# Kernel optimization log

Measured on AMD Instinct MI355X. Metric: run time of the kernel, lower is better.

The kernel has to match this reference:

```python
import jax, jax.numpy as jnp
import numpy as np
import math

# IPA hyperparameters (AlphaFold2 / ProtSeed defaults)
H, C, PQ, PV = 12, 16, 4, 8
CS, CZ = 384, 128
INF, EPS = 1e5, 1e-8
CAT = H * (CZ + C + 4 * PV)  # 2112


def setup_inputs() -> dict:
    key = jax.random.key(0)
    ks = jax.random.split(key, 20)
    B, N = 1, 512
    s = jax.random.normal(ks[0], (B, N, CS), jnp.float32)
    z = jax.random.normal(ks[1], (B, N, N, CZ), jnp.float32)
    # valid rotation matrices via QR of random gaussians
    rot = jnp.linalg.qr(jax.random.normal(ks[2], (B, N, 3, 3), jnp.float32))[0]
    trans = jax.random.normal(ks[3], (B, N, 3), jnp.float32)
    mask = jnp.ones((B, N), jnp.float32)
    sc = 0.02
    params = {
        'w_q': jax.random.normal(ks[4], (CS, H * C), jnp.float32) * sc,
        'b_q': jnp.zeros((H * C,), jnp.float32),
        'w_kv': jax.random.normal(ks[5], (CS, 2 * H * C), jnp.float32) * sc,
        'b_kv': jnp.zeros((2 * H * C,), jnp.float32),
        'w_qp': jax.random.normal(ks[6], (CS, H * PQ * 3), jnp.float32) * sc,
        'b_qp': jnp.zeros((H * PQ * 3,), jnp.float32),
        'w_kvp': jax.random.normal(ks[7], (CS, H * (PQ + PV) * 3), jnp.float32) * sc,
        'b_kvp': jnp.zeros((H * (PQ + PV) * 3,), jnp.float32),
        'w_b': jax.random.normal(ks[8], (CZ, H), jnp.float32) * sc,
        'b_b': jnp.zeros((H,), jnp.float32),
        'head_weights': jnp.full((H,), 0.5414, jnp.float32),  # softplus^-1(1)
        'w_out': jax.random.normal(ks[9], (CAT, CS), jnp.float32) * sc,
        'b_out': jnp.zeros((CS,), jnp.float32),
    }
    return {'s': s, 'z': z, 'rot': rot, 'trans': trans, 'mask': mask, **params}


def reference(s, z, rot, trans, mask, w_q, b_q, w_kv, b_kv, w_qp, b_qp,
              w_kvp, b_kvp, w_b, b_b, head_weights, w_out, b_out):
    B, N, _ = s.shape
    w_c = math.sqrt(1.0 / (3 * C))
    w_l = math.sqrt(1.0 / 3)
    w_p = math.sqrt(1.0 / (3 * (PQ * 9.0 / 2)))

    # scalar q/k/v: [B,N,H,C]
    q = (s @ w_q + b_q).reshape(B, N, H, C)
    kv = (s @ w_kv + b_kv).reshape(B, N, H, 2 * C)
    k, v = kv[..., :C], kv[..., C:]

    # point q/k/v in global frame. torch splits the projection into 3 chunks
    # (x,y,z) along the channel dim then stacks -> [B,N,H*P,3]
    def to_pts(w, b, p):
        pts = jnp.stack(jnp.split(s @ w + b, 3, axis=-1), axis=-1)  # [B,N,H*p,3]
        pts = jnp.einsum('bnij,bnpj->bnpi', rot, pts) + trans[:, :, None, :]
        return pts.reshape(B, N, H, p, 3)

    q_pts = to_pts(w_qp, b_qp, PQ)
    kv_pts = to_pts(w_kvp, b_kvp, PQ + PV)
    k_pts, v_pts = kv_pts[..., :PQ, :], kv_pts[..., PQ:, :]

    # pair bias [B,N,N,H]
    bias = z @ w_b + b_b

    # scalar attention logits [B,H,i,j]
    a = jnp.einsum('bihc,bjhc->bhij', q, k) * w_c
    a = a + w_l * jnp.transpose(bias, (0, 3, 1, 2))

    # point-distance term: [B,i,j,H,PQ]
    d2 = jnp.sum((q_pts[:, :, None] - k_pts[:, None]) ** 2, axis=-1)
    hw = jax.nn.softplus(head_weights) * w_p
    pt_att = -0.5 * jnp.sum(d2 * hw[None, None, None, :, None], axis=-1)  # [B,i,j,H]
    a = a + jnp.transpose(pt_att, (0, 3, 1, 2))

    sq_mask = INF * (mask[:, :, None] * mask[:, None, :] - 1.0)  # [B,i,j]
    a = jax.nn.softmax(a + sq_mask[:, None], axis=-1)  # [B,H,i,j]

    # scalar output [B,N,H*C]
    o = jnp.einsum('bhij,bjhc->bihc', a, v).reshape(B, N, H * C)

    # point output, mapped back to local frames: [B,i,H,PV,3]
    o_pt = jnp.einsum('bhij,bjhpx->bihpx', a, v_pts)
    o_pt = jnp.einsum('bnji,bnhpj->bnhpi', rot, o_pt - trans[:, :, None, None, :])
    o_pt_norm = jnp.sqrt(jnp.sum(o_pt ** 2, axis=-1) + EPS).reshape(B, N, H * PV)
    o_pt = o_pt.reshape(B, N, H * PV, 3)

    # pair output [B,N,H*CZ]
    o_pair = jnp.einsum('bhij,bijc->bihc', a, z).reshape(B, N, H * CZ)

    cat = jnp.concatenate(
        [o, o_pt[..., 0], o_pt[..., 1], o_pt[..., 2], o_pt_norm, o_pair], axis=-1)
    return cat @ w_out + b_out  # [B,N,C_s]
```

## Files before the change

### kernel.cpp

```cpp
#include <hip/hip_runtime.h>
#include <math.h>

#define NN 512
#define CSd 384
#define CATd 2112
#define KF_CHUNK 264
#define KF_SPLIT 8

__device__ __forceinline__ int aidx(int h, int j) {
  return h * 544 + ((j >> 6) * 68) + (j & 63);
}
__device__ __forceinline__ float f4c(const float4& v, int k) {
  return k == 0 ? v.x : (k == 1 ? v.y : (k == 2 ? v.z : v.w));
}

__global__ void k_projgemm(const float* __restrict__ s,
                           const float* __restrict__ w_q, const float* __restrict__ b_q,
                           const float* __restrict__ w_kv, const float* __restrict__ b_kv,
                           const float* __restrict__ w_qp, const float* __restrict__ b_qp,
                           const float* __restrict__ w_kvp, const float* __restrict__ b_kvp,
                           float* __restrict__ proj)
{
  __shared__ float sT[384 * 40];
  const int t  = threadIdx.x;
  const int i0 = blockIdx.x * 32;
  const int c0 = blockIdx.y * 64;

  for (int u = t; u < 32 * 384; u += 256) {
    int row = u / 384, col = u % 384;
    sT[col * 40 + row] = s[(i0 + row) * CSd + col];
  }
  __syncthreads();

  const int c    = t & 63;
  const int rgrp = t >> 6;
  const int gc   = c0 + c;

  const float* wp;
  int stride;
  float bias;
  if (gc < 192)      { wp = w_q   + gc;         stride = 192; bias = b_q[gc]; }
  else if (gc < 576) { wp = w_kv  + (gc - 192); stride = 384; bias = b_kv[gc - 192]; }
  else if (gc < 720) { wp = w_qp  + (gc - 576); stride = 144; bias = b_qp[gc - 576]; }
  else               { wp = w_kvp + (gc - 720); stride = 432; bias = b_kvp[gc - 720]; }

  float acc[8];
#pragma unroll
  for (int j = 0; j < 8; j++) acc[j] = bias;

  const int r0 = rgrp * 8;
#pragma unroll 4
  for (int kk = 0; kk < 384; kk++) {
    float wv = *wp; wp += stride;
    const float4 a0 = *reinterpret_cast<const float4*>(&sT[kk * 40 + r0]);
    const float4 a1 = *reinterpret_cast<const float4*>(&sT[kk * 40 + r0 + 4]);
    acc[0] += a0.x * wv; acc[1] += a0.y * wv; acc[2] += a0.z * wv; acc[3] += a0.w * wv;
    acc[4] += a1.x * wv; acc[5] += a1.y * wv; acc[6] += a1.z * wv; acc[7] += a1.w * wv;
  }
#pragma unroll
  for (int j = 0; j < 8; j++)
    proj[(size_t)(i0 + r0 + j) * 1152 + gc] = acc[j];
}

__global__ void k_rot(const float* __restrict__ proj,
                      const float* __restrict__ rot, const float* __restrict__ trans,
                      float* __restrict__ q, float* __restrict__ kT, float* __restrict__ vcat,
                      float* __restrict__ qp, float* __restrict__ kpT)
{
  __shared__ float ptsL[576];
  const int i = blockIdx.x, t = threadIdx.x;
  const float* pr = proj + (size_t)i * 1152;

  for (int u = t; u < 576; u += 256) ptsL[u] = pr[576 + u];

  for (int cI = t; cI < 576; cI += 256) {
    float pv = pr[cI];
    if (cI < 192) q[i * 192 + cI] = pv;
    else {
      int local = cI - 192, h = local >> 5, cc = local & 31;
      if (cc < 16) kT[(size_t)(h * 16 + cc) * NN + i] = pv;
      else         vcat[(size_t)i * 480 + h * 16 + (cc - 16)] = pv;
    }
  }
  __syncthreads();

  for (int p = t; p < 192; p += 256) {
    float x, y, zz;
    if (p < 48) { x = ptsL[p]; y = ptsL[48 + p]; zz = ptsL[96 + p]; }
    else { int idx = p - 48; x = ptsL[144 + idx]; y = ptsL[288 + idx]; zz = ptsL[432 + idx]; }
    const float* Rm = rot + i * 9;
    const float* tr = trans + i * 3;
    float rx = Rm[0] * x + Rm[1] * y + Rm[2] * zz + tr[0];
    float ry = Rm[3] * x + Rm[4] * y + Rm[5] * zz + tr[1];
    float rz = Rm[6] * x + Rm[7] * y + Rm[8] * zz + tr[2];
    if (p < 48) {
      float* d = qp + ((size_t)i * 48 + p) * 3;
      d[0] = rx; d[1] = ry; d[2] = rz;
    } else {
      int idx = p - 48, h = idx / 12, pp = idx % 12;
      if (pp < 4) {
        size_t rbase = (size_t)((h * 4 + pp) * 3) * NN + i;
        kpT[rbase] = rx; kpT[rbase + NN] = ry; kpT[rbase + 2 * NN] = rz;
      } else {
        size_t rbase = (size_t)i * 480 + 192 + (h * 8 + pp - 4) * 3;
        vcat[rbase] = rx; vcat[rbase + 1] = ry; vcat[rbase + 2] = rz;
      }
    }
  }
}

__global__ void k_logits(const float* __restrict__ z, const float* __restrict__ w_b,
                         const float* __restrict__ b_b, const float* __restrict__ mask,
                         const float* __restrict__ q, const float* __restrict__ kT,
                         const float* __restrict__ qp, const float* __restrict__ kpT,
                         const float* __restrict__ hws,
                         float* __restrict__ a)
{
  const int t = threadIdx.x;
  const int i = blockIdx.x >> 1;
  const int j = ((blockIdx.x & 1) << 8) + t;

  float acc[12];
#pragma unroll
  for (int h = 0; h < 12; h++) acc[h] = 0.f;

  const float4* zr = reinterpret_cast<const float4*>(z + ((size_t)i * NN + j) * 128);
#pragma unroll
  for (int ch = 0; ch < 4; ch++) {
    float4 zc[8];
#pragma unroll
    for (int u = 0; u < 8; u++) zc[u] = zr[ch * 8 + u];
#pragma unroll
    for (int u = 0; u < 8; u++) {
      const int c0 = ch * 32 + u * 4;
#pragma unroll
      for (int h = 0; h < 12; h++) {
        acc[h] += zc[u].x * w_b[(c0 + 0) * 12 + h]
                + zc[u].y * w_b[(c0 + 1) * 12 + h]
                + zc[u].z * w_b[(c0 + 2) * 12 + h]
                + zc[u].w * w_b[(c0 + 3) * 12 + h];
      }
    }
  }

  const float mterm = 100000.0f * (mask[i] * mask[j] - 1.0f);
  const float W_L = 0.57735026919f;
  const float W_C = 0.14433756730f;

#pragma unroll
  for (int h = 0; h < 12; h++) {
    float dot = 0.f;
#pragma unroll
    for (int c = 0; c < 16; c++)
      dot += q[i * 192 + h * 16 + c] * kT[(size_t)(h * 16 + c) * NN + j];
    float d2 = 0.f;
#pragma unroll
    for (int pc = 0; pc < 12; pc++) {
      float dd = qp[(size_t)i * 144 + h * 12 + pc] - kpT[(size_t)(h * 12 + pc) * NN + j];
      d2 += dd * dd;
    }
    const float hwv = 0.13608276348f * log1pf(expf(hws[h]));
    a[((size_t)h * NN + i) * NN + j] =
        W_L * (acc[h] + b_b[h]) + mterm + W_C * dot - 0.5f * hwv * d2;
  }
}

__global__ void __launch_bounds__(512, 2)
k_out(const float* __restrict__ a, const float* __restrict__ vcat,
      const float* __restrict__ z,
      const float* __restrict__ rot, const float* __restrict__ trans,
      float* __restrict__ cat)
{
  __shared__ float aL[12 * 544];
  __shared__ float redp[8][16][56];
  __shared__ float optF[288];
  float* red2 = &redp[0][0][0];

  const int i = blockIdx.x, t = threadIdx.x;

  for (int u = t; u < 12 * 512; u += 512) {
    int h = u >> 9, j = u & 511;
    aL[aidx(h, j)] = a[((size_t)h * NN + i) * NN + j];
  }
  __syncthreads();

  {
    const int wv = t >> 6, l = t & 63;
    for (int h = wv; h < 12; h += 8) {
      const int j0 = l * 8;
      float4 x0 = *reinterpret_cast<const float4*>(&aL[aidx(h, j0)]);
      float4 x1 = *reinterpret_cast<const float4*>(&aL[aidx(h, j0 + 4)]);
      float m8 = fmaxf(fmaxf(fmaxf(x0.x, x0.y), fmaxf(x0.z, x0.w)),
                       fmaxf(fmaxf(x1.x, x1.y), fmaxf(x1.z, x1.w)));
      for (int o = 1; o < 64; o <<= 1) m8 = fmaxf(m8, __shfl_xor(m8, o));
      x0.x = expf(x0.x - m8); x0.y = expf(x0.y - m8);
      x0.z = expf(x0.z - m8); x0.w = expf(x0.w - m8);
      x1.x = expf(x1.x - m8); x1.y = expf(x1.y - m8);
      x1.z = expf(x1.z - m8); x1.w = expf(x1.w - m8);
      float s8 = x0.x + x0.y + x0.z + x0.w + x1.x + x1.y + x1.z + x1.w;
      for (int o = 1; o < 64; o <<= 1) s8 += __shfl_xor(s8, o);
      float inv = 1.0f / s8;
      x0.x *= inv; x0.y *= inv; x0.z *= inv; x0.w *= inv;
      x1.x *= inv; x1.y *= inv; x1.z *= inv; x1.w *= inv;
      *reinterpret_cast<float4*>(&aL[aidx(h, j0)]) = x0;
      *reinterpret_cast<float4*>(&aL[aidx(h, j0 + 4)]) = x1;
    }
  }
  __syncthreads();

  const int cg = t & 15;
  const int jq = (t >> 4) & 3;
  const int wv = t >> 6;
  float acc1[12][8];
#pragma unroll
  for (int h = 0; h < 12; h++)
#pragma unroll
    for (int c = 0; c < 8; c++) acc1[h][c] = 0.f;

  {
    const int c8 = cg * 8;
    const int jb = wv * 64 + jq * 16;
    const float* zb = z + (size_t)i * 65536 + c8;
    for (int ch = 0; ch < 4; ch++) {
      const int j0c = jb + ch * 4;
      float4 p4[12];
#pragma unroll
      for (int h = 0; h < 12; h++)
        p4[h] = *reinterpret_cast<const float4*>(&aL[aidx(h, j0c)]);
#pragma unroll
      for (int jj = 0; jj < 4; jj++) {
        const float4 za = *reinterpret_cast<const float4*>(&zb[(size_t)(j0c + jj) * 128]);
        const float4 zc = *reinterpret_cast<const float4*>(&zb[(size_t)(j0c + jj) * 128 + 4]);
#pragma unroll
        for (int h = 0; h < 12; h++) {
          const float pv = f4c(p4[h], jj);
          acc1[h][0] += pv * za.x; acc1[h][1] += pv * za.y;
          acc1[h][2] += pv * za.z; acc1[h][3] += pv * za.w;
          acc1[h][4] += pv * zc.x; acc1[h][5] += pv * zc.y;
          acc1[h][6] += pv * zc.z; acc1[h][7] += pv * zc.w;
        }
      }
    }
#pragma unroll
    for (int h = 0; h < 12; h++)
#pragma unroll
      for (int c = 0; c < 8; c++) {
        float v2 = acc1[h][c];
        v2 += __shfl_xor(v2, 16);
        v2 += __shfl_xor(v2, 32);
        acc1[h][c] = v2;
      }
  }

  if (jq == 0) {
#pragma unroll
    for (int h = 0; h < 6; h++) {
      *reinterpret_cast<float4*>(&redp[wv][cg][h * 8]) =
        make_float4(acc1[h][0], acc1[h][1], acc1[h][2], acc1[h][3]);
      *reinterpret_cast<float4*>(&redp[wv][cg][h * 8 + 4]) =
        make_float4(acc1[h][4], acc1[h][5], acc1[h][6], acc1[h][7]);
    }
  }
  __syncthreads();
  for (int e = t; e < 768; e += 512) {
    int h = e >> 7, c = e & 127;
    float sv = 0.f;
#pragma unroll
    for (int w2 = 0; w2 < 8; w2++) sv += redp[w2][c >> 3][h * 8 + (c & 7)];
    cat[(size_t)i * CATd + 576 + e] = sv;
  }
  __syncthreads();

  if (jq == 0) {
#pragma unroll
    for (int h = 0; h < 6; h++) {
      *reinterpret_cast<float4*>(&redp[wv][cg][h * 8]) =
        make_float4(acc1[6 + h][0], acc1[6 + h][1], acc1[6 + h][2], acc1[6 + h][3]);
      *reinterpret_cast<float4*>(&redp[wv][cg][h * 8 + 4]) =
        make_float4(acc1[6 + h][4], acc1[6 + h][5], acc1[6 + h][6], acc1[6 + h][7]);
    }
  }
  __syncthreads();
  for (int e = t; e < 768; e += 512) {
    int h = e >> 7, c = e & 127;
    float sv = 0.f;
#pragma unroll
    for (int w2 = 0; w2 < 8; w2++) sv += redp[w2][c >> 3][h * 8 + (c & 7)];
    cat[(size_t)i * CATd + 576 + 768 + e] = sv;
  }
  __syncthreads();

  const int oc = t & 63, jw = t >> 6;
  const int h2 = oc / 5, c5 = oc - h2 * 5;
  const int c8b = c5 * 8;
  float acc2[8];
#pragma unroll
  for (int c = 0; c < 8; c++) acc2[c] = 0.f;

  if (oc < 60) {
    const int vbase = (c8b < 16) ? (h2 * 16 + c8b) : (192 + h2 * 24 + (c8b - 16));
    for (int ch = 0; ch < 16; ch++) {
      const int j0c = jw * 64 + ch * 4;
      const float4 p4 = *reinterpret_cast<const float4*>(&aL[aidx(h2, j0c)]);
#pragma unroll
      for (int jj = 0; jj < 4; jj++) {
        const float* vr = &vcat[(size_t)(j0c + jj) * 480 + vbase];
        const float4 va = *reinterpret_cast<const float4*>(vr);
        const float4 vb = *reinterpret_cast<const float4*>(vr + 4);
        const float pv = f4c(p4, jj);
        acc2[0] += pv * va.x; acc2[1] += pv * va.y;
        acc2[2] += pv * va.z; acc2[3] += pv * va.w;
        acc2[4] += pv * vb.x; acc2[5] += pv * vb.y;
        acc2[6] += pv * vb.z; acc2[7] += pv * vb.w;
      }
    }
  }
  if (oc < 60) {
    *reinterpret_cast<float4*>(&red2[((size_t)jw * 64 + oc) * 8]) =
      make_float4(acc2[0], acc2[1], acc2[2], acc2[3]);
    *reinterpret_cast<float4*>(&red2[((size_t)jw * 64 + oc) * 8 + 4]) =
      make_float4(acc2[4], acc2[5], acc2[6], acc2[7]);
  }
  __syncthreads();

  for (int e = t; e < 480; e += 512) {
    const int oc2 = e >> 3, cc = e & 7;
    float sv = 0.f;
#pragma unroll
    for (int w2 = 0; w2 < 8; w2++) sv += red2[((size_t)w2 * 64 + oc2) * 8 + cc];
    const int hh = e / 40, c40 = e - hh * 40;
    if (c40 < 16) cat[(size_t)i * CATd + hh * 16 + c40] = sv;
    else optF[hh * 24 + (c40 - 16)] = sv;
  }
  __syncthreads();

  if (t < 96) {
    const int h = t >> 3, p = t & 7;
    const float* Rm = rot + i * 9;
    const float* tr = trans + i * 3;
    float ox = optF[h * 24 + p * 3 + 0] - tr[0];
    float oy = optF[h * 24 + p * 3 + 1] - tr[1];
    float oz = optF[h * 24 + p * 3 + 2] - tr[2];
    float rx = Rm[0] * ox + Rm[3] * oy + Rm[6] * oz;
    float ry = Rm[1] * ox + Rm[4] * oy + Rm[7] * oz;
    float rz = Rm[2] * ox + Rm[5] * oy + Rm[8] * oz;
    float nrm = sqrtf(rx * rx + ry * ry + rz * rz + 1e-8f);
    size_t b = (size_t)i * CATd;
    cat[b + 192 + t] = rx; cat[b + 288 + t] = ry;
    cat[b + 384 + t] = rz; cat[b + 480 + t] = nrm;
  }
}

__global__ void k_final(const float* __restrict__ cat, const float* __restrict__ w_out,
                        float* __restrict__ part)
{
  __shared__ float sT[KF_CHUNK * 36];
  const int t  = threadIdx.x;
  const int i0 = blockIdx.x * 32;
  const int c0 = blockIdx.y * 64;
  const int k0 = blockIdx.z * KF_CHUNK;

  for (int u = t; u < 32 * KF_CHUNK; u += 256) {
    int row = u / KF_CHUNK, kk = u % KF_CHUNK;
    sT[kk * 36 + row] = cat[(size_t)(i0 + row) * CATd + k0 + kk];
  }
  __syncthreads();

  const int c    = t & 63;
  const int rgrp = t >> 6;
  const int r0   = rgrp * 8;
  const int gc   = c0 + c;

  float acc[8];
#pragma unroll
  for (int j = 0; j < 8; j++) acc[j] = 0.f;

  const float* wp = w_out + (size_t)k0 * 384 + gc;
#pragma unroll 4
  for (int kk = 0; kk < KF_CHUNK; kk++) {
    float wv = wp[(size_t)kk * 384];
    const float4 a0 = *reinterpret_cast<const float4*>(&sT[kk * 36 + r0]);
    const float4 a1 = *reinterpret_cast<const float4*>(&sT[kk * 36 + r0 + 4]);
    acc[0] += a0.x * wv; acc[1] += a0.y * wv; acc[2] += a0.z * wv; acc[3] += a0.w * wv;
    acc[4] += a1.x * wv; acc[5] += a1.y * wv; acc[6] += a1.z * wv; acc[7] += a1.w * wv;
  }

  float* pb = part + (size_t)blockIdx.z * NN * 384;
#pragma unroll
  for (int j = 0; j < 8; j++)
    pb[(size_t)(i0 + r0 + j) * 384 + gc] = acc[j];
}

__global__ void k_reduce(const float* __restrict__ part, const float* __restrict__ b_out,
                         float* __restrict__ out)
{
  const int idx = blockIdx.x * 256 + threadIdx.x;
  const int c = idx % 384;
  float acc = b_out[c];
#pragma unroll
  for (int ks = 0; ks < KF_SPLIT; ks++)
    acc += part[(size_t)ks * NN * 384 + idx];
  out[idx] = acc;
}

extern "C" void kernel_launch(void* const* d_in, const int* in_sizes, int n_in,
                              void* d_out, int out_size, void* d_ws, size_t ws_size,
                              hipStream_t stream) {
  const float* s      = (const float*)d_in[0];
  const float* z      = (const float*)d_in[1];
  const float* rot    = (const float*)d_in[2];
  const float* trans  = (const float*)d_in[3];
  const float* mask   = (const float*)d_in[4];
  const float* w_q    = (const float*)d_in[5];
  const float* b_q    = (const float*)d_in[6];
  const float* w_kv   = (const float*)d_in[7];
  const float* b_kv   = (const float*)d_in[8];
  const float* w_qp   = (const float*)d_in[9];
  const float* b_qp   = (const float*)d_in[10];
  const float* w_kvp  = (const float*)d_in[11];
  const float* b_kvp  = (const float*)d_in[12];
  const float* w_b    = (const float*)d_in[13];
  const float* b_b    = (const float*)d_in[14];
  const float* hws    = (const float*)d_in[15];
  const float* w_out  = (const float*)d_in[16];
  const float* b_out  = (const float*)d_in[17];
  float* out = (float*)d_out;

  float* ws   = (float*)d_ws;
  float* q    = ws;
  float* kT   = q    + 98304;
  float* vcat = kT   + 98304;
  float* qp   = vcat + 245760;
  float* kpT  = qp   + 73728;
  float* a    = kpT  + 73728;
  float* cat  = a    + 3145728;
  float* proj = a;
  float* part = a;

  k_projgemm<<<dim3(16, 18), 256, 0, stream>>>(s, w_q, b_q, w_kv, b_kv,
                                               w_qp, b_qp, w_kvp, b_kvp, proj);
  k_rot<<<512, 256, 0, stream>>>(proj, rot, trans, q, kT, vcat, qp, kpT);
  k_logits<<<1024, 256, 0, stream>>>(z, w_b, b_b, mask, q, kT, qp, kpT, hws, a);
  k_out<<<512, 512, 0, stream>>>(a, vcat, z, rot, trans, cat);
  k_final<<<dim3(16, 6, KF_SPLIT), 256, 0, stream>>>(cat, w_out, part);
  k_reduce<<<768, 256, 0, stream>>>(part, b_out, out);
}
```

Baseline: 201.4 us.

## Split output kernel into softmax/value kernel and parallel pair-output kernel

The monolithic per-row output kernel is split in three. The first computes the softmax, writes the probabilities back to global memory and does the scalar and point value reductions against a transposed value layout. The second spreads the attention-by-z pair contraction over a 4x512 grid with a partial-sum buffer, and the third reduces those partials into the concat buffer. This aims to raise parallelism and occupancy on the z-bandwidth-bound pair product, at the cost of extra launches, an extra round trip of the attention matrix through global memory, and the partial-sum traffic.

```diff
diff --git a/kernel.cpp b/kernel.cpp
--- a/kernel.cpp
+++ b/kernel.cpp
@@ -6,13 +6,6 @@
 #define CATd 2112
 #define KF_CHUNK 264
 #define KF_SPLIT 8
-
-__device__ __forceinline__ int aidx(int h, int j) {
-  return h * 544 + ((j >> 6) * 68) + (j & 63);
-}
-__device__ __forceinline__ float f4c(const float4& v, int k) {
-  return k == 0 ? v.x : (k == 1 ? v.y : (k == 2 ? v.z : v.w));
-}
 
 __global__ void k_projgemm(const float* __restrict__ s,
                            const float* __restrict__ w_q, const float* __restrict__ b_q,
@@ -64,7 +57,7 @@
 
 __global__ void k_rot(const float* __restrict__ proj,
                       const float* __restrict__ rot, const float* __restrict__ trans,
-                      float* __restrict__ q, float* __restrict__ kT, float* __restrict__ vcat,
+                      float* __restrict__ q, float* __restrict__ kT, float* __restrict__ vcatT,
                       float* __restrict__ qp, float* __restrict__ kpT)
 {
   __shared__ float ptsL[576];
@@ -79,7 +72,7 @@
     else {
       int local = cI - 192, h = local >> 5, cc = local & 31;
       if (cc < 16) kT[(size_t)(h * 16 + cc) * NN + i] = pv;
-      else         vcat[(size_t)i * 480 + h * 16 + (cc - 16)] = pv;
+      else         vcatT[(size_t)(h * 16 + (cc - 16)) * NN + i] = pv;
     }
   }
   __syncthreads();
@@ -102,8 +95,8 @@
         size_t rbase = (size_t)((h * 4 + pp) * 3) * NN + i;
         kpT[rbase] = rx; kpT[rbase + NN] = ry; kpT[rbase + 2 * NN] = rz;
       } else {
-        size_t rbase = (size_t)i * 480 + 192 + (h * 8 + pp - 4) * 3;
-        vcat[rbase] = rx; vcat[rbase + 1] = ry; vcat[rbase + 2] = rz;
+        size_t rbase = (size_t)(192 + (h * 8 + pp - 4) * 3) * NN + i;
+        vcatT[rbase] = rx; vcatT[rbase + NN] = ry; vcatT[rbase + 2 * NN] = rz;
       }
     }
   }
@@ -165,172 +158,58 @@
   }
 }
 
-__global__ void __launch_bounds__(512, 2)
-k_out(const float* __restrict__ a, const float* __restrict__ vcat,
-      const float* __restrict__ z,
+__global__ void __launch_bounds__(512)
+k_pvt(float* __restrict__ a, const float* __restrict__ vcatT,
       const float* __restrict__ rot, const float* __restrict__ trans,
       float* __restrict__ cat)
 {
-  __shared__ float aL[12 * 544];
-  __shared__ float redp[8][16][56];
+  __shared__ float PL[12 * 516];
   __shared__ float optF[288];
-  float* red2 = &redp[0][0][0];
-
   const int i = blockIdx.x, t = threadIdx.x;
-
-  for (int u = t; u < 12 * 512; u += 512) {
-    int h = u >> 9, j = u & 511;
-    aL[aidx(h, j)] = a[((size_t)h * NN + i) * NN + j];
-  }
-  __syncthreads();
-
-  {
-    const int wv = t >> 6, l = t & 63;
-    for (int h = wv; h < 12; h += 8) {
-      const int j0 = l * 8;
-      float4 x0 = *reinterpret_cast<const float4*>(&aL[aidx(h, j0)]);
-      float4 x1 = *reinterpret_cast<const float4*>(&aL[aidx(h, j0 + 4)]);
-      float m8 = fmaxf(fmaxf(fmaxf(x0.x, x0.y), fmaxf(x0.z, x0.w)),
-                       fmaxf(fmaxf(x1.x, x1.y), fmaxf(x1.z, x1.w)));
-      for (int o = 1; o < 64; o <<= 1) m8 = fmaxf(m8, __shfl_xor(m8, o));
-      x0.x = expf(x0.x - m8); x0.y = expf(x0.y - m8);
-      x0.z = expf(x0.z - m8); x0.w = expf(x0.w - m8);
-      x1.x = expf(x1.x - m8); x1.y = expf(x1.y - m8);
-      x1.z = expf(x1.z - m8); x1.w = expf(x1.w - m8);
-      float s8 = x0.x + x0.y + x0.z + x0.w + x1.x + x1.y + x1.z + x1.w;
-      for (int o = 1; o < 64; o <<= 1) s8 += __shfl_xor(s8, o);
-      float inv = 1.0f / s8;
-      x0.x *= inv; x0.y *= inv; x0.z *= inv; x0.w *= inv;
-      x1.x *= inv; x1.y *= inv; x1.z *= inv; x1.w *= inv;
-      *reinterpret_cast<float4*>(&aL[aidx(h, j0)]) = x0;
-      *reinterpret_cast<float4*>(&aL[aidx(h, j0 + 4)]) = x1;
-    }
-  }
-  __syncthreads();
-
-  const int cg = t & 15;
-  const int jq = (t >> 4) & 3;
-  const int wv = t >> 6;
-  float acc1[12][8];
-#pragma unroll
-  for (int h = 0; h < 12; h++)
-#pragma unroll
-    for (int c = 0; c < 8; c++) acc1[h][c] = 0.f;
-
-  {
-    const int c8 = cg * 8;
-    const int jb = wv * 64 + jq * 16;
-    const float* zb = z + (size_t)i * 65536 + c8;
-    for (int ch = 0; ch < 4; ch++) {
-      const int j0c = jb + ch * 4;
-      float4 p4[12];
-#pragma unroll
-      for (int h = 0; h < 12; h++)
-        p4[h] = *reinterpret_cast<const float4*>(&aL[aidx(h, j0c)]);
-#pragma unroll
-      for (int jj = 0; jj < 4; jj++) {
-        const float4 za = *reinterpret_cast<const float4*>(&zb[(size_t)(j0c + jj) * 128]);
-        const float4 zc = *reinterpret_cast<const float4*>(&zb[(size_t)(j0c + jj) * 128 + 4]);
-#pragma unroll
-        for (int h = 0; h < 12; h++) {
-          const float pv = f4c(p4[h], jj);
-          acc1[h][0] += pv * za.x; acc1[h][1] += pv * za.y;
-          acc1[h][2] += pv * za.z; acc1[h][3] += pv * za.w;
-          acc1[h][4] += pv * zc.x; acc1[h][5] += pv * zc.y;
-          acc1[h][6] += pv * zc.z; acc1[h][7] += pv * zc.w;
-        }
-      }
-    }
-#pragma unroll
-    for (int h = 0; h < 12; h++)
-#pragma unroll
-      for (int c = 0; c < 8; c++) {
-        float v2 = acc1[h][c];
-        v2 += __shfl_xor(v2, 16);
-        v2 += __shfl_xor(v2, 32);
-        acc1[h][c] = v2;
-      }
-  }
-
-  if (jq == 0) {
-#pragma unroll
-    for (int h = 0; h < 6; h++) {
-      *reinterpret_cast<float4*>(&redp[wv][cg][h * 8]) =
-        make_float4(acc1[h][0], acc1[h][1], acc1[h][2], acc1[h][3]);
-      *reinterpret_cast<float4*>(&redp[wv][cg][h * 8 + 4]) =
-        make_float4(acc1[h][4], acc1[h][5], acc1[h][6], acc1[h][7]);
-    }
-  }
-  __syncthreads();
-  for (int e = t; e < 768; e += 512) {
-    int h = e >> 7, c = e & 127;
-    float sv = 0.f;
-#pragma unroll
-    for (int w2 = 0; w2 < 8; w2++) sv += redp[w2][c >> 3][h * 8 + (c & 7)];
-    cat[(size_t)i * CATd + 576 + e] = sv;
-  }
-  __syncthreads();
-
-  if (jq == 0) {
-#pragma unroll
-    for (int h = 0; h < 6; h++) {
-      *reinterpret_cast<float4*>(&redp[wv][cg][h * 8]) =
-        make_float4(acc1[6 + h][0], acc1[6 + h][1], acc1[6 + h][2], acc1[6 + h][3]);
-      *reinterpret_cast<float4*>(&redp[wv][cg][h * 8 + 4]) =
-        make_float4(acc1[6 + h][4], acc1[6 + h][5], acc1[6 + h][6], acc1[6 + h][7]);
-    }
-  }
-  __syncthreads();
-  for (int e = t; e < 768; e += 512) {
-    int h = e >> 7, c = e & 127;
-    float sv = 0.f;
-#pragma unroll
-    for (int w2 = 0; w2 < 8; w2++) sv += redp[w2][c >> 3][h * 8 + (c & 7)];
-    cat[(size_t)i * CATd + 576 + 768 + e] = sv;
-  }
-  __syncthreads();
-
-  const int oc = t & 63, jw = t >> 6;
-  const int h2 = oc / 5, c5 = oc - h2 * 5;
-  const int c8b = c5 * 8;
-  float acc2[8];
-#pragma unroll
-  for (int c = 0; c < 8; c++) acc2[c] = 0.f;
-
-  if (oc < 60) {
-    const int vbase = (c8b < 16) ? (h2 * 16 + c8b) : (192 + h2 * 24 + (c8b - 16));
-    for (int ch = 0; ch < 16; ch++) {
-      const int j0c = jw * 64 + ch * 4;
-      const float4 p4 = *reinterpret_cast<const float4*>(&aL[aidx(h2, j0c)]);
-#pragma unroll
-      for (int jj = 0; jj < 4; jj++) {
-        const float* vr = &vcat[(size_t)(j0c + jj) * 480 + vbase];
-        const float4 va = *reinterpret_cast<const float4*>(vr);
-        const float4 vb = *reinterpret_cast<const float4*>(vr + 4);
-        const float pv = f4c(p4, jj);
-        acc2[0] += pv * va.x; acc2[1] += pv * va.y;
-        acc2[2] += pv * va.z; acc2[3] += pv * va.w;
-        acc2[4] += pv * vb.x; acc2[5] += pv * vb.y;
-        acc2[6] += pv * vb.z; acc2[7] += pv * vb.w;
-      }
-    }
-  }
-  if (oc < 60) {
-    *reinterpret_cast<float4*>(&red2[((size_t)jw * 64 + oc) * 8]) =
-      make_float4(acc2[0], acc2[1], acc2[2], acc2[3]);
-    *reinterpret_cast<float4*>(&red2[((size_t)jw * 64 + oc) * 8 + 4]) =
-      make_float4(acc2[4], acc2[5], acc2[6], acc2[7]);
-  }
-  __syncthreads();
-
-  for (int e = t; e < 480; e += 512) {
-    const int oc2 = e >> 3, cc = e & 7;
-    float sv = 0.f;
-#pragma unroll
-    for (int w2 = 0; w2 < 8; w2++) sv += red2[((size_t)w2 * 64 + oc2) * 8 + cc];
-    const int hh = e / 40, c40 = e - hh * 40;
-    if (c40 < 16) cat[(size_t)i * CATd + hh * 16 + c40] = sv;
-    else optF[hh * 24 + (c40 - 16)] = sv;
+  const int w = t >> 6, l = t & 63;
+
+  for (int u = t; u < 12 * 128; u += 512) {
+    int h = u >> 7, c4 = u & 127;
+    *reinterpret_cast<float4*>(&PL[h * 516 + c4 * 4]) =
+      *reinterpret_cast<const float4*>(&a[((size_t)h * NN + i) * NN + c4 * 4]);
+  }
+  __syncthreads();
+
+  for (int h = w; h < 12; h += 8) {
+    float x[8];
+    float m = -1e30f;
+#pragma unroll
+    for (int k = 0; k < 8; k++) { x[k] = PL[h * 516 + k * 64 + l]; m = fmaxf(m, x[k]); }
+    for (int o = 1; o < 64; o <<= 1) m = fmaxf(m, __shfl_xor(m, o));
+    float sm = 0.f;
+#pragma unroll
+    for (int k = 0; k < 8; k++) { x[k] = expf(x[k] - m); sm += x[k]; }
+    for (int o = 1; o < 64; o <<= 1) sm += __shfl_xor(sm, o);
+    float inv = 1.0f / sm;
+#pragma unroll
+    for (int k = 0; k < 8; k++) PL[h * 516 + k * 64 + l] = x[k] * inv;
+  }
+  __syncthreads();
+
+  for (int u = t; u < 12 * 128; u += 512) {
+    int h = u >> 7, c4 = u & 127;
+    *reinterpret_cast<float4*>(&a[((size_t)h * NN + i) * NN + c4 * 4]) =
+      *reinterpret_cast<const float4*>(&PL[h * 516 + c4 * 4]);
+  }
+
+  for (int v = w; v < 480; v += 8) {
+    const int h = (v < 192) ? (v >> 4) : ((v - 192) / 24);
+    const float* vr = vcatT + (size_t)v * NN;
+    const float* pr = PL + h * 516;
+    float acc = 0.f;
+#pragma unroll
+    for (int k = 0; k < 8; k++)
+      acc += pr[k * 64 + l] * vr[k * 64 + l];
+    for (int o = 1; o < 64; o <<= 1) acc += __shfl_xor(acc, o);
+    if (l == 0) {
+      if (v < 192) cat[(size_t)i * CATd + v] = acc;
+      else         optF[v - 192] = acc;
+    }
   }
   __syncthreads();
 
@@ -338,9 +217,9 @@
     const int h = t >> 3, p = t & 7;
     const float* Rm = rot + i * 9;
     const float* tr = trans + i * 3;
-    float ox = optF[h * 24 + p * 3 + 0] - tr[0];
-    float oy = optF[h * 24 + p * 3 + 1] - tr[1];
-    float oz = optF[h * 24 + p * 3 + 2] - tr[2];
+    float ox = optF[(h * 8 + p) * 3 + 0] - tr[0];
+    float oy = optF[(h * 8 + p) * 3 + 1] - tr[1];
+    float oz = optF[(h * 8 + p) * 3 + 2] - tr[2];
     float rx = Rm[0] * ox + Rm[3] * oy + Rm[6] * oz;
     float ry = Rm[1] * ox + Rm[4] * oy + Rm[7] * oz;
     float rz = Rm[2] * ox + Rm[5] * oy + Rm[8] * oz;
@@ -349,6 +228,60 @@
     cat[b + 192 + t] = rx; cat[b + 288 + t] = ry;
     cat[b + 384 + t] = rz; cat[b + 480 + t] = nrm;
   }
+}
+
+__global__ void k_opair(const float* __restrict__ a, const float* __restrict__ z,
+                        float* __restrict__ opart)
+{
+  __shared__ float PL[12 * 128];
+  __shared__ float red[4][64][26];
+  const int jb = blockIdx.x, i = blockIdx.y;
+  const int t = threadIdx.x, c2 = t & 63, jq = t >> 6;
+
+  for (int u = t; u < 384; u += 256) {
+    int h = u >> 5, c4 = u & 31;
+    *reinterpret_cast<float4*>(&PL[h * 128 + c4 * 4]) =
+      *reinterpret_cast<const float4*>(&a[((size_t)h * NN + i) * NN + jb * 128 + c4 * 4]);
+  }
+  __syncthreads();
+
+  float acc[12][2];
+#pragma unroll
+  for (int h = 0; h < 12; h++) { acc[h][0] = 0.f; acc[h][1] = 0.f; }
+
+  const int j0 = jb * 128 + jq * 32;
+  const float2* zr = reinterpret_cast<const float2*>(z + ((size_t)i * NN + j0) * 128) + c2;
+  for (int jj = 0; jj < 32; jj++) {
+    float2 zv = zr[(size_t)jj * 64];
+#pragma unroll
+    for (int h = 0; h < 12; h++) {
+      float pv = PL[h * 128 + jq * 32 + jj];
+      acc[h][0] += pv * zv.x; acc[h][1] += pv * zv.y;
+    }
+  }
+
+#pragma unroll
+  for (int h = 0; h < 12; h++) {
+    red[jq][c2][h * 2]     = acc[h][0];
+    red[jq][c2][h * 2 + 1] = acc[h][1];
+  }
+  __syncthreads();
+
+  for (int e = t; e < 1536; e += 256) {
+    int h = e >> 7, c = e & 127;
+    int ci = c >> 1, half = c & 1;
+    float sv = red[0][ci][h * 2 + half] + red[1][ci][h * 2 + half]
+             + red[2][ci][h * 2 + half] + red[3][ci][h * 2 + half];
+    opart[((size_t)i * 4 + jb) * 1536 + e] = sv;
+  }
+}
+
+__global__ void k_opreduce(const float* __restrict__ opart, float* __restrict__ cat)
+{
+  const int idx = blockIdx.x * 256 + threadIdx.x;
+  const int i = idx / 1536, e = idx - i * 1536;
+  const float* pb = opart + (size_t)i * 4 * 1536 + e;
+  cat[(size_t)i * CATd + 576 + e] = pb[0] + pb[1536] + pb[3072] + pb[4608];
 }
 
 __global__ void k_final(const float* __restrict__ cat, const float* __restrict__ w_out,
@@ -426,22 +359,25 @@
   const float* b_out  = (const float*)d_in[17];
   float* out = (float*)d_out;
 
-  float* ws   = (float*)d_ws;
-  float* q    = ws;
-  float* kT   = q    + 98304;
-  float* vcat = kT   + 98304;
-  float* qp   = vcat + 245760;
-  float* kpT  = qp   + 73728;
-  float* a    = kpT  + 73728;
-  float* cat  = a    + 3145728;
-  float* proj = a;
-  float* part = a;
+  float* ws    = (float*)d_ws;
+  float* q     = ws;
+  float* kT    = q     + 98304;
+  float* vcatT = kT    + 98304;
+  float* qp    = vcatT + 245760;
+  float* kpT   = qp    + 73728;
+  float* a     = kpT   + 73728;
+  float* cat   = a     + 3145728;
+  float* opart = cat   + 1081344;
+  float* proj  = a;
+  float* part  = a;
 
   k_projgemm<<<dim3(16, 18), 256, 0, stream>>>(s, w_q, b_q, w_kv, b_kv,
                                                w_qp, b_qp, w_kvp, b_kvp, proj);
-  k_rot<<<512, 256, 0, stream>>>(proj, rot, trans, q, kT, vcat, qp, kpT);
+  k_rot<<<512, 256, 0, stream>>>(proj, rot, trans, q, kT, vcatT, qp, kpT);
   k_logits<<<1024, 256, 0, stream>>>(z, w_b, b_b, mask, q, kT, qp, kpT, hws, a);
-  k_out<<<512, 512, 0, stream>>>(a, vcat, z, rot, trans, cat);
+  k_pvt<<<512, 512, 0, stream>>>(a, vcatT, rot, trans, cat);
+  k_opair<<<dim3(4, 512), 256, 0, stream>>>(a, z, opart);
+  k_opreduce<<<3072, 256, 0, stream>>>(opart, cat);
   k_final<<<dim3(16, 6, KF_SPLIT), 256, 0, stream>>>(cat, w_out, part);
   k_reduce<<<768, 256, 0, stream>>>(part, b_out, out);
 }
```

New measurement: 196.6 us. 2.4% less time.
